# Optimization experiments

Measured on AMD Instinct MI355X. Metric: run time of the kernel, lower is better.

Reference implementation:

```python
import jax, jax.numpy as jnp
import numpy as np

COMMITMENT_COST = 0.25
NUM_EMBEDDINGS = 1024
EMBEDDING_DIM = 256


def setup_inputs() -> dict:
    key = jax.random.key(0)
    k1, k2 = jax.random.split(key)
    inputs = jax.random.normal(k1, (64, 256, 32, 32), dtype=jnp.float32)
    emb_w = jax.random.normal(k2, (NUM_EMBEDDINGS, EMBEDDING_DIM), dtype=jnp.float32)
    return {"inputs": inputs, "emb_w": emb_w}


def reference(inputs, emb_w):
    # NCHW -> NHWC, flatten to [N, D]
    x = jnp.transpose(inputs, (0, 2, 3, 1))  # [B, H, W, D]
    B, H, W, D = x.shape
    flat = x.reshape(-1, D)  # [N, D]

    distances = (
        jnp.sum(flat * flat, axis=1, keepdims=True)
        + jnp.sum(emb_w * emb_w, axis=1)
        - 2.0 * flat @ emb_w.T
    )
    idx = jnp.argmin(distances, axis=1)  # [N]

    # one-hot @ W is just a gather of codebook rows
    quantized = emb_w[idx].reshape(B, H, W, D)

    # avg_probs = mean of one-hot encodings = normalized codeword counts
    counts = jnp.zeros((NUM_EMBEDDINGS,), dtype=jnp.float32).at[idx].add(1.0)
    avg_probs = counts / flat.shape[0]
    perplexity = jnp.exp(-jnp.sum(avg_probs * jnp.log(avg_probs + 1e-10)))

    e_latent_loss = jnp.mean((jax.lax.stop_gradient(quantized) - x) ** 2)
    loss = COMMITMENT_COST * e_latent_loss

    # straight-through estimator
    quantized_st = x + jax.lax.stop_gradient(quantized - x)
    quantized_out = jnp.transpose(quantized_st, (0, 3, 1, 2))  # back to NCHW

    return loss, quantized_out, perplexity, idx.reshape(B, H, W)
```

## Files before the change

### kernel.cpp

```cpp
#include <hip/hip_runtime.h>
#include <hip/hip_bf16.h>
#include <math.h>

typedef _Float16 f16;
typedef __attribute__((ext_vector_type(8))) _Float16 f16x8;
typedef __attribute__((ext_vector_type(16))) float f32x16;

#define DIMS 256
#define NCODE 1024
#define NPTS 65536

#define OUT_Q_OFF 1
#define OUT_PERP_OFF 16777217
#define OUT_IDX_OFF 16777218

#define EHI_F32_OFF 4
#define ELO_F32_OFF (4 + 131072)
#define TILE_BYTES 16384

#define XSTRIDE 132

__device__ __forceinline__ void gload_lds16(const void* g, void* l) {
    __builtin_amdgcn_global_load_lds(
        (const __attribute__((address_space(1))) unsigned int*)g,
        (__attribute__((address_space(3))) unsigned int*)l, 16, 0, 0);
}

__global__ __launch_bounds__(256) void k_eprep(const float* __restrict__ ew,
                                               char* __restrict__ ehi,
                                               char* __restrict__ elo,
                                               float* __restrict__ enorm) {
    int w = threadIdx.x >> 6;
    int l = threadIdx.x & 63;
    int row = blockIdx.x * 4 + w;
    float4 v = *reinterpret_cast<const float4*>(ew + (size_t)row * DIMS + l * 4);
    float vv[4] = {v.x, v.y, v.z, v.w};
    __align__(8) f16 hh[4];
    __align__(8) f16 ll[4];
    float s = 0.0f;
    #pragma unroll
    for (int e = 0; e < 4; ++e) {
        f16 h = (f16)vv[e];
        hh[e] = h;
        ll[e] = (f16)(vv[e] - (float)h);
        s += vv[e] * vv[e];
    }
    size_t off = (size_t)(row >> 5) * TILE_BYTES + (size_t)(row & 31) * 512
               + (size_t)((((l >> 1) ^ (row & 7)) << 4) + ((l & 1) << 3));
    *reinterpret_cast<float2*>(ehi + off) = *reinterpret_cast<float2*>(hh);
    *reinterpret_cast<float2*>(elo + off) = *reinterpret_cast<float2*>(ll);
    #pragma unroll
    for (int off2 = 32; off2 > 0; off2 >>= 1) s += __shfl_down(s, off2);
    if (l == 0) enorm[row] = s;
}

__global__ __launch_bounds__(256, 2) void k_argmin_mfma(const float* __restrict__ x,
                                                        const char* __restrict__ ehi,
                                                        const char* __restrict__ elo,
                                                        const float* __restrict__ enorm,
                                                        int* __restrict__ out_idx) {
    __shared__ __align__(16) char smem[2 * 2 * TILE_BYTES];
    __shared__ float enorm_lds[NCODE];
    float* Xs = (float*)smem;

    const int t = threadIdx.x;
    const int wave = t >> 6;
    const int lane = t & 63;
    const int lrow = lane & 31;
    const int lhalf = lane >> 5;

    const int blk = blockIdx.x;
    const int b = blk >> 3;
    const int hw0 = (blk & 7) << 7;
    const float* xb = x + (size_t)b * (DIMS * 1024) + hw0;

    #pragma unroll
    for (int i = 0; i < 4; ++i) enorm_lds[t + 256 * i] = enorm[t + 256 * i];

    f16x8 ahi[16], alo[16];
    #pragma unroll
    for (int dc = 0; dc < 4; ++dc) {
        __syncthreads();
        #pragma unroll
        for (int i = 0; i < 8; ++i) {
            int d = (t >> 5) + 8 * i;
            int p4 = (t & 31) * 4;
            float4 v = *reinterpret_cast<const float4*>(xb + (size_t)(dc * 64 + d) * 1024 + p4);
            *reinterpret_cast<float4*>(&Xs[d * XSTRIDE + p4]) = v;
        }
        __syncthreads();
        int p = wave * 32 + lrow;
        #pragma unroll
        for (int kcl = 0; kcl < 4; ++kcl) {
            f16x8 h, l;
            #pragma unroll
            for (int e = 0; e < 8; ++e) {
                float xv = Xs[(kcl * 16 + lhalf * 8 + e) * XSTRIDE + p];
                f16 hi = (f16)xv;
                h[e] = hi;
                l[e] = (f16)(xv - (float)hi);
            }
            ahi[dc * 4 + kcl] = h;
            alo[dc * 4 + kcl] = l;
        }
    }
    __syncthreads();

    const char* gplane = (wave >> 1) ? elo : ehi;
    const int pl_off = (wave >> 1) * TILE_BYTES;
    const int woff = (wave & 1) * 8192;

    #pragma unroll
    for (int i = 0; i < 8; ++i) {
        int off = woff + i * 1024;
        gload_lds16(gplane + off + lane * 16, smem + pl_off + off);
    }
    __syncthreads();

    float bestv[16];
    int besti[16];
    #pragma unroll
    for (int r = 0; r < 16; ++r) { bestv[r] = 3.4e38f; besti[r] = 0; }

    int cur = 0;
    for (int rd = 0; rd < 32; ++rd) {
        if (rd + 1 < 32) {
            const char* gp = gplane + (size_t)(rd + 1) * TILE_BYTES;
            char* lp = smem + (cur ^ 1) * (2 * TILE_BYTES) + pl_off;
            #pragma unroll
            for (int i = 0; i < 8; ++i) {
                int off = woff + i * 1024;
                gload_lds16(gp + off + lane * 16, lp + off);
            }
        }

        const char* EHb = smem + cur * (2 * TILE_BYTES);
        const char* ELb = EHb + TILE_BYTES;
        f32x16 acc0, acc1;
        #pragma unroll
        for (int r = 0; r < 16; ++r) { acc0[r] = 0.0f; acc1[r] = 0.0f; }

        #pragma unroll
        for (int kc = 0; kc < 16; ++kc) {
            int g = kc * 2 + lhalf;
            int ra = lrow * 512 + ((g ^ (lrow & 7)) << 4);
            f16x8 bh = *reinterpret_cast<const f16x8*>(EHb + ra);
            f16x8 bl = *reinterpret_cast<const f16x8*>(ELb + ra);
            acc0 = __builtin_amdgcn_mfma_f32_32x32x16_f16(ahi[kc], bh, acc0, 0, 0, 0);
            acc1 = __builtin_amdgcn_mfma_f32_32x32x16_f16(ahi[kc], bl, acc1, 0, 0, 0);
            if (kc & 1)
                acc1 = __builtin_amdgcn_mfma_f32_32x32x16_f16(alo[kc], bh, acc1, 0, 0, 0);
            else
                acc0 = __builtin_amdgcn_mfma_f32_32x32x16_f16(alo[kc], bh, acc0, 0, 0, 0);
        }

        const int code0 = rd * 32;
        float en = enorm_lds[code0 + lrow];
        int cw = code0 + lrow;
        #pragma unroll
        for (int r = 0; r < 16; ++r) {
            float s = fmaf(-2.0f, acc0[r] + acc1[r], en);
            if (s < bestv[r]) { bestv[r] = s; besti[r] = cw; }
        }

        __syncthreads();
        cur ^= 1;
    }

    #pragma unroll
    for (int off = 1; off <= 16; off <<= 1) {
        #pragma unroll
        for (int r = 0; r < 16; ++r) {
            float ov = __shfl_xor(bestv[r], off);
            int oi = __shfl_xor(besti[r], off);
            if (ov < bestv[r] || (ov == bestv[r] && oi < besti[r])) {
                bestv[r] = ov;
                besti[r] = oi;
            }
        }
    }
    if (lrow == 0) {
        #pragma unroll
        for (int r = 0; r < 16; ++r) {
            int row = (r & 3) + 8 * (r >> 2) + 4 * lhalf;
            out_idx[blk * 128 + wave * 32 + row] = besti[r];
        }
    }
}

#define QSTRIDE 258
__global__ __launch_bounds__(512) void k_quant(const float* __restrict__ x,
                                               const float* __restrict__ ew,
                                               const int* __restrict__ idxv,
                                               float* __restrict__ out,
                                               float* __restrict__ loss_acc,
                                               int* __restrict__ counts) {
    __shared__ float Eq[64 * QSTRIDE];
    __shared__ int ids[64];
    __shared__ int h[NCODE];
    const int t = threadIdx.x;
    const int blk = blockIdx.x;
    const int b = blk >> 4;
    const int hw0 = (blk & 15) << 6;

    if (t < 64) ids[t] = idxv[(b << 10) + hw0 + t];
    h[t] = 0;
    h[t + 512] = 0;
    __syncthreads();

    if (t < 64) atomicAdd(&h[ids[t]], 1);

    #pragma unroll
    for (int i = 0; i < 8; ++i) {
        int f = i * 512 + t;
        int row = f >> 6;
        int c4 = f & 63;
        float4 v = *reinterpret_cast<const float4*>(ew + (size_t)ids[row] * DIMS + c4 * 4);
        float2 lo2 = {v.x, v.y};
        float2 hi2 = {v.z, v.w};
        *reinterpret_cast<float2*>(&Eq[row * QSTRIDE + c4 * 4]) = lo2;
        *reinterpret_cast<float2*>(&Eq[row * QSTRIDE + c4 * 4 + 2]) = hi2;
    }
    __syncthreads();

    const int p = t & 63;
    const int c0 = t >> 6;
    float lsum = 0.0f;
    #pragma unroll
    for (int k = 0; k < 32; ++k) {
        int c = k * 8 + c0;
        unsigned g = ((unsigned)b << 18) | ((unsigned)c << 10) | (unsigned)(hw0 + p);
        float xv = x[g];
        float q = Eq[p * QSTRIDE + c];
        float d = q - xv;
        out[OUT_Q_OFF + g] = xv + d;
        lsum += d * d;
    }
    #pragma unroll
    for (int off = 32; off > 0; off >>= 1) lsum += __shfl_down(lsum, off);
    if ((t & 63) == 0) atomicAdd(&loss_acc[blk & 63], lsum);

    int v0 = h[t];
    if (v0) atomicAdd(&counts[t], v0);
    int v1 = h[t + 512];
    if (v1) atomicAdd(&counts[t + 512], v1);
    if (t < 64) out[OUT_IDX_OFF + (b << 10) + hw0 + t] = (float)ids[t];
}

__global__ __launch_bounds__(256) void k_final(const int* __restrict__ counts,
                                               const float* __restrict__ loss_acc,
                                               float* __restrict__ out) {
    int t = threadIdx.x;
    float s = 0.0f;
    #pragma unroll
    for (int i = 0; i < 4; ++i) {
        int cnt = counts[t + 256 * i];
        float p = (float)cnt * (1.0f / 65536.0f);
        s += p * logf(p + 1e-10f);
    }
    #pragma unroll
    for (int off = 32; off > 0; off >>= 1) s += __shfl_down(s, off);
    __shared__ float wsum[4];
    if ((t & 63) == 0) wsum[t >> 6] = s;
    __syncthreads();
    if (t == 0) {
        float S = wsum[0] + wsum[1] + wsum[2] + wsum[3];
        out[OUT_PERP_OFF] = expf(-S);
        float ls = 0.0f;
        for (int i = 0; i < 64; ++i) ls += loss_acc[i];
        out[0] = 0.25f * (ls * (1.0f / 16777216.0f));
    }
}

extern "C" void kernel_launch(void* const* d_in, const int* in_sizes, int n_in,
                              void* d_out, int out_size, void* d_ws, size_t ws_size,
                              hipStream_t stream) {
    const float* x = (const float*)d_in[0];
    const float* ew = (const float*)d_in[1];
    float* out = (float*)d_out;
    float* ws = (float*)d_ws;

    float* loss_acc = ws;
    int* counts = (int*)(ws + 64);
    float* enorm = ws + 64 + 1024;
    int* idxv = (int*)(ws + 64 + 2048);

    char* ehi = (char*)(out + EHI_F32_OFF);
    char* elo = (char*)(out + ELO_F32_OFF);

    hipMemsetAsync(d_ws, 0, (64 + 1024) * sizeof(float), stream);

    k_eprep<<<256, 256, 0, stream>>>(ew, ehi, elo, enorm);
    k_argmin_mfma<<<512, 256, 0, stream>>>(x, ehi, elo, enorm, idxv);
    k_quant<<<1024, 512, 0, stream>>>(x, ew, idxv, out, loss_acc, counts);
    k_final<<<1, 256, 0, stream>>>(counts, loss_acc, out);
}
```

Baseline: 176.7 us.

## Software-pipeline argmin epilogue behind next round's MFMAs and vectorize gather loads

The distance kernel now uses two alternating accumulators, so the argmin update for the previous 32-code round runs after the current round's MFMA chain. This lets the compare work overlap with matrix-core execution. It also merges the two split accumulators into one serial MFMA chain and raises wave priority around the MFMA block with s_setprio. The quantize/gather kernel switches from scalar x loads to float4 loads of four consecutive spatial points per thread. Stores remain scalar because the output offset of 1 breaks alignment. The single accumulator chain lengthens the MFMA dependency chain, and the extra accumulator raises register pressure.

```diff
diff --git a/kernel.cpp b/kernel.cpp
--- a/kernel.cpp
+++ b/kernel.cpp
@@ -122,50 +122,63 @@
     #pragma unroll
     for (int r = 0; r < 16; ++r) { bestv[r] = 3.4e38f; besti[r] = 0; }
 
-    int cur = 0;
-    for (int rd = 0; rd < 32; ++rd) {
-        if (rd + 1 < 32) {
-            const char* gp = gplane + (size_t)(rd + 1) * TILE_BYTES;
-            char* lp = smem + (cur ^ 1) * (2 * TILE_BYTES) + pl_off;
-            #pragma unroll
-            for (int i = 0; i < 8; ++i) {
-                int off = woff + i * 1024;
-                gload_lds16(gp + off + lane * 16, lp + off);
-            }
-        }
-
-        const char* EHb = smem + cur * (2 * TILE_BYTES);
-        const char* ELb = EHb + TILE_BYTES;
-        f32x16 acc0, acc1;
-        #pragma unroll
-        for (int r = 0; r < 16; ++r) { acc0[r] = 0.0f; acc1[r] = 0.0f; }
-
-        #pragma unroll
-        for (int kc = 0; kc < 16; ++kc) {
-            int g = kc * 2 + lhalf;
-            int ra = lrow * 512 + ((g ^ (lrow & 7)) << 4);
-            f16x8 bh = *reinterpret_cast<const f16x8*>(EHb + ra);
-            f16x8 bl = *reinterpret_cast<const f16x8*>(ELb + ra);
-            acc0 = __builtin_amdgcn_mfma_f32_32x32x16_f16(ahi[kc], bh, acc0, 0, 0, 0);
-            acc1 = __builtin_amdgcn_mfma_f32_32x32x16_f16(ahi[kc], bl, acc1, 0, 0, 0);
-            if (kc & 1)
-                acc1 = __builtin_amdgcn_mfma_f32_32x32x16_f16(alo[kc], bh, acc1, 0, 0, 0);
-            else
-                acc0 = __builtin_amdgcn_mfma_f32_32x32x16_f16(alo[kc], bh, acc0, 0, 0, 0);
-        }
-
-        const int code0 = rd * 32;
-        float en = enorm_lds[code0 + lrow];
-        int cw = code0 + lrow;
+#define ROUND_BODY(ACC_CUR, ACC_PREV, RD)                                         \
+    {                                                                             \
+        const int rd_ = (RD);                                                     \
+        const int cur_ = rd_ & 1;                                                 \
+        if (rd_ + 1 < 32) {                                                       \
+            const char* gp_ = gplane + (size_t)(rd_ + 1) * TILE_BYTES;            \
+            char* lp_ = smem + (cur_ ^ 1) * (2 * TILE_BYTES) + pl_off;            \
+            _Pragma("unroll")                                                     \
+            for (int i_ = 0; i_ < 8; ++i_) {                                      \
+                int off_ = woff + i_ * 1024;                                      \
+                gload_lds16(gp_ + off_ + lane * 16, lp_ + off_);                  \
+            }                                                                     \
+        }                                                                         \
+        const char* EHb_ = smem + cur_ * (2 * TILE_BYTES);                        \
+        const char* ELb_ = EHb_ + TILE_BYTES;                                     \
+        _Pragma("unroll")                                                         \
+        for (int r_ = 0; r_ < 16; ++r_) ACC_CUR[r_] = 0.0f;                       \
+        __builtin_amdgcn_s_setprio(1);                                            \
+        _Pragma("unroll")                                                         \
+        for (int kc_ = 0; kc_ < 16; ++kc_) {                                      \
+            int g_ = kc_ * 2 + lhalf;                                             \
+            int ra_ = lrow * 512 + ((g_ ^ (lrow & 7)) << 4);                      \
+            f16x8 bh_ = *reinterpret_cast<const f16x8*>(EHb_ + ra_);              \
+            f16x8 bl_ = *reinterpret_cast<const f16x8*>(ELb_ + ra_);              \
+            ACC_CUR = __builtin_amdgcn_mfma_f32_32x32x16_f16(ahi[kc_], bh_, ACC_CUR, 0, 0, 0); \
+            ACC_CUR = __builtin_amdgcn_mfma_f32_32x32x16_f16(ahi[kc_], bl_, ACC_CUR, 0, 0, 0); \
+            ACC_CUR = __builtin_amdgcn_mfma_f32_32x32x16_f16(alo[kc_], bh_, ACC_CUR, 0, 0, 0); \
+        }                                                                         \
+        __builtin_amdgcn_s_setprio(0);                                            \
+        if (rd_ > 0) {                                                            \
+            const int pc0_ = (rd_ - 1) * 32;                                      \
+            float en_ = enorm_lds[pc0_ + lrow];                                   \
+            int cw_ = pc0_ + lrow;                                                \
+            _Pragma("unroll")                                                     \
+            for (int r_ = 0; r_ < 16; ++r_) {                                     \
+                float s_ = fmaf(-2.0f, ACC_PREV[r_], en_);                        \
+                if (s_ < bestv[r_]) { bestv[r_] = s_; besti[r_] = cw_; }          \
+            }                                                                     \
+        }                                                                         \
+        __syncthreads();                                                          \
+    }
+
+    f32x16 accA, accB;
+    for (int rr = 0; rr < 16; ++rr) {
+        ROUND_BODY(accA, accB, 2 * rr);
+        ROUND_BODY(accB, accA, 2 * rr + 1);
+    }
+    {
+        float en = enorm_lds[31 * 32 + lrow];
+        int cw = 31 * 32 + lrow;
         #pragma unroll
         for (int r = 0; r < 16; ++r) {
-            float s = fmaf(-2.0f, acc0[r] + acc1[r], en);
+            float s = fmaf(-2.0f, accB[r], en);
             if (s < bestv[r]) { bestv[r] = s; besti[r] = cw; }
         }
-
-        __syncthreads();
-        cur ^= 1;
-    }
+    }
+#undef ROUND_BODY
 
     #pragma unroll
     for (int off = 1; off <= 16; off <<= 1) {
@@ -223,18 +236,25 @@
     }
     __syncthreads();
 
-    const int p = t & 63;
-    const int c0 = t >> 6;
+    const int q4 = t & 15;
+    const int cb = t >> 4;
+    const int p = q4 * 4;
     float lsum = 0.0f;
     #pragma unroll
-    for (int k = 0; k < 32; ++k) {
-        int c = k * 8 + c0;
+    for (int k = 0; k < 8; ++k) {
+        int c = k * 32 + cb;
         unsigned g = ((unsigned)b << 18) | ((unsigned)c << 10) | (unsigned)(hw0 + p);
-        float xv = x[g];
-        float q = Eq[p * QSTRIDE + c];
-        float d = q - xv;
-        out[OUT_Q_OFF + g] = xv + d;
-        lsum += d * d;
+        float4 xv = *reinterpret_cast<const float4*>(x + g);
+        float q0 = Eq[(p + 0) * QSTRIDE + c];
+        float q1 = Eq[(p + 1) * QSTRIDE + c];
+        float q2 = Eq[(p + 2) * QSTRIDE + c];
+        float q3 = Eq[(p + 3) * QSTRIDE + c];
+        float d0 = q0 - xv.x, d1 = q1 - xv.y, d2 = q2 - xv.z, d3 = q3 - xv.w;
+        out[OUT_Q_OFF + g + 0] = xv.x + d0;
+        out[OUT_Q_OFF + g + 1] = xv.y + d1;
+        out[OUT_Q_OFF + g + 2] = xv.z + d2;
+        out[OUT_Q_OFF + g + 3] = xv.w + d3;
+        lsum += d0 * d0 + d1 * d1 + d2 * d2 + d3 * d3;
     }
     #pragma unroll
     for (int off = 32; off > 0; off >>= 1) lsum += __shfl_down(lsum, off);
```

After: 173.4 us. No clear change (-1.9%).
